# Kernel optimization log

Hardware: AMD Instinct MI355X
Metric: run time of the kernel (lower is better)

The kernel has to match this reference:

```python
import jax, jax.numpy as jnp
import numpy as np

N, E, D, R = 50000, 600000, 128, 500


def setup_inputs() -> dict:
    key = jax.random.key(0)
    ks = jax.random.split(key, 9)
    h = jax.random.normal(ks[0], (N, D), dtype=jnp.float32)
    norm = jax.random.uniform(ks[1], (N, 1), dtype=jnp.float32)
    emb_rel = jax.random.normal(ks[2], (R, D), dtype=jnp.float32)
    scale = 1.0 / np.sqrt(D)  # xavier-ish scale for DxD weights
    weight_neighbor = jax.random.normal(ks[3], (D, D), dtype=jnp.float32) * scale
    loop_weight = jax.random.normal(ks[4], (D, D), dtype=jnp.float32) * scale
    evolve_loop_weight = jax.random.normal(ks[5], (D, D), dtype=jnp.float32) * scale
    src = jax.random.randint(ks[6], (E,), 0, N, dtype=jnp.int32)
    dst = jax.random.randint(ks[7], (E,), 0, N, dtype=jnp.int32)
    etype = jax.random.randint(ks[8], (E,), 0, R, dtype=jnp.int32)
    return {
        "h": h, "norm": norm, "emb_rel": emb_rel,
        "weight_neighbor": weight_neighbor, "loop_weight": loop_weight,
        "evolve_loop_weight": evolve_loop_weight,
        "src": src, "dst": dst, "etype": etype,
    }


def reference(h, norm, emb_rel, weight_neighbor, loop_weight,
              evolve_loop_weight, src, dst, etype):
    # msg_func: gather src node features + relation embeddings, add, dense matmul
    msg = (h[src] + emb_rel[etype]) @ weight_neighbor        # [E, D]
    # update_all(fn.sum): scatter-sum messages into destination nodes
    agg = jax.ops.segment_sum(msg, dst, num_segments=N)       # [N, D]
    # apply_func: scale by per-node norm
    h_agg = agg * norm                                        # [N, D]
    # self-loop: nodes with in-degree > 0 use loop_weight, others evolve_loop_weight
    in_deg = jax.ops.segment_sum(jnp.ones((E,), dtype=jnp.float32), dst,
                                 num_segments=N)              # [N]
    loop_msg = jnp.where((in_deg > 0)[:, None],
                         h @ loop_weight,
                         h @ evolve_loop_weight)              # [N, D]
    node_repr = h_agg + loop_msg
    return jax.nn.relu(node_repr)
```

## Files before the change

### kernel.cpp

```cpp
#include <hip/hip_runtime.h>
#include <hip/hip_bf16.h>


#define DIM 128
#define MAXD 64

typedef __attribute__((ext_vector_type(8))) short bf16x8_t;
typedef __attribute__((ext_vector_type(4))) float f32x4_t;

__device__ inline ushort f2bf(float f) {
    __hip_bfloat16 b = __float2bfloat16(f);
    return *reinterpret_cast<ushort*>(&b);
}
__device__ inline float blo(unsigned u) { return __uint_as_float(u << 16); }
__device__ inline float bhi(unsigned u) { return __uint_as_float(u & 0xffff0000u); }
__device__ inline uint4 cvt8(const float4& a, const float4& b) {
    uint4 o;
    o.x = f2bf(a.x) | ((unsigned)f2bf(a.y) << 16);
    o.y = f2bf(a.z) | ((unsigned)f2bf(a.w) << 16);
    o.z = f2bf(b.x) | ((unsigned)f2bf(b.y) << 16);
    o.w = f2bf(b.z) | ((unsigned)f2bf(b.w) << 16);
    return o;
}

__global__ __launch_bounds__(256) void init_kernel(
    const float4* __restrict__ h4, const float4* __restrict__ emb4,
    const float* __restrict__ Wn, const float* __restrict__ Wl,
    uint4* __restrict__ h8, uint4* __restrict__ emb8,
    ushort* __restrict__ Bpack, int* __restrict__ cursor,
    int* __restrict__ zcount, int nH, int nE, int N, int R)
{
    int i = blockIdx.x * 256 + threadIdx.x;
    if (i < nH) {
        int per = (N + 1) * 2;
        int s = i / per, rem = i - s * per;
        int n = rem >> 1, hh = rem & 1;
        h8[i] = (n == N) ? make_uint4(0, 0, 0, 0)
                         : cvt8(h4[n * 32 + s * 4 + hh * 2],
                                h4[n * 32 + s * 4 + hh * 2 + 1]);
        return;
    }
    int j = i - nH;
    if (j < nE) {
        int per = (R + 1) * 2;
        int s = j / per, rem = j - s * per;
        int n = rem >> 1, hh = rem & 1;
        emb8[j] = (n == R) ? make_uint4(0, 0, 0, 0)
                           : cvt8(emb4[n * 32 + s * 4 + hh * 2],
                                  emb4[n * 32 + s * 4 + hh * 2 + 1]);
        return;
    }
    j -= nE;
    if (j < 32768) {
        int jj   = j & 7;
        int lane = (j >> 3) & 63;
        int ks   = (j >> 9) & 7;
        int nt   = j >> 12;
        int k = ks * 32 + (lane >> 4) * 8 + jj;
        int n = nt * 16 + (lane & 15);
        float v = (k < DIM) ? Wn[k * DIM + n] : Wl[(k - DIM) * DIM + n];
        Bpack[j] = f2bf(v);
        return;
    }
    j -= 32768;
    if (j < N) { cursor[j] = 0; return; }
    if (j == N) *zcount = 0;
}

__global__ __launch_bounds__(256) void fill_kernel(
    const int4* __restrict__ src4, const int4* __restrict__ dst4,
    const int4* __restrict__ et4, int* __restrict__ cursor,
    unsigned* __restrict__ region, int E4,
    const int* __restrict__ src, const int* __restrict__ dst,
    const int* __restrict__ etype, int E)
{
    int i = blockIdx.x * 256 + threadIdx.x;
    if (i < E4) {
        int4 s = src4[i], d = dst4[i], t = et4[i];
        int p;
        p = atomicAdd(cursor + d.x, 1);
        region[d.x * MAXD + p] = (unsigned)s.x | ((unsigned)t.x << 17);
        p = atomicAdd(cursor + d.y, 1);
        region[d.y * MAXD + p] = (unsigned)s.y | ((unsigned)t.y << 17);
        p = atomicAdd(cursor + d.z, 1);
        region[d.z * MAXD + p] = (unsigned)s.z | ((unsigned)t.z << 17);
        p = atomicAdd(cursor + d.w, 1);
        region[d.w * MAXD + p] = (unsigned)s.w | ((unsigned)t.w << 17);
    }
    if (i == 0)
        for (int e = E4 * 4; e < E; ++e) {
            int p = atomicAdd(cursor + dst[e], 1);
            region[dst[e] * MAXD + p] = (unsigned)src[e] | ((unsigned)etype[e] << 17);
        }
}

__device__ inline void addbf8(float* a, uint4 hv, uint4 rv) {
    a[0] += blo(hv.x) + blo(rv.x); a[1] += bhi(hv.x) + bhi(rv.x);
    a[2] += blo(hv.y) + blo(rv.y); a[3] += bhi(hv.y) + bhi(rv.y);
    a[4] += blo(hv.z) + blo(rv.z); a[5] += bhi(hv.z) + bhi(rv.z);
    a[6] += blo(hv.w) + blo(rv.w); a[7] += bhi(hv.w) + bhi(rv.w);
}

__global__ __launch_bounds__(256) void gather_kernel(
    const uint4* __restrict__ h8,
    const uint4* __restrict__ e8,
    const float* __restrict__ norm,
    const int* __restrict__ cursor,
    const unsigned* __restrict__ region,
    uint4* __restrict__ aggn8,
    int* __restrict__ zcount, int* __restrict__ zlist,
    int N, int R, unsigned SENT)
{
    __shared__ uint4 embS[1024];

    int s  = blockIdx.x & 7;
    int nb = blockIdx.x >> 3;

    const uint4* esrc = e8 + (size_t)s * (R + 1) * 2;
    int nse = (R + 1) * 2;
    if (nse > 1024) nse = 1024;
    for (int idx = threadIdx.x; idx < nse; idx += 256)
        embS[idx] = esrc[idx];
    __syncthreads();

    int n = nb * 128 + (threadIdx.x >> 1);
    if (n >= N) return;
    int l = threadIdx.x & 1;
    int cnt = cursor[n];
    uint4* aout = aggn8 + ((size_t)s * N + n) * 2 + l;

    if (cnt == 0) {
        if (s == 0 && l == 0) { int p = atomicAdd(zcount, 1); zlist[p] = n; }
        *aout = make_uint4(0, 0, 0, 0);
        return;
    }

    const uint4* hsl = h8 + (size_t)s * (N + 1) * 2 + l;
    const uint4* el  = embS + l;
    const unsigned* reg = region + (size_t)n * MAXD;
    float nm = norm[n];
    float a[8] = {0.f, 0.f, 0.f, 0.f, 0.f, 0.f, 0.f, 0.f};

    uint4 r = *(const uint4*)reg;
    for (int k = 0; k < cnt; k += 4) {
        int kp = (k + 4 < MAXD - 3) ? (k + 4) : (MAXD - 4);
        uint4 rn = *(const uint4*)(reg + kp);
        unsigned w0 = r.x;
        unsigned w1 = (k + 1 < cnt) ? r.y : SENT;
        unsigned w2 = (k + 2 < cnt) ? r.z : SENT;
        unsigned w3 = (k + 3 < cnt) ? r.w : SENT;
        uint4 h0 = hsl[(w0 & 0x1FFFF) * 2];
        uint4 h1 = hsl[(w1 & 0x1FFFF) * 2];
        uint4 h2 = hsl[(w2 & 0x1FFFF) * 2];
        uint4 h3 = hsl[(w3 & 0x1FFFF) * 2];
        uint4 e0 = el[(w0 >> 17) * 2];
        uint4 e1 = el[(w1 >> 17) * 2];
        uint4 e2 = el[(w2 >> 17) * 2];
        uint4 e3 = el[(w3 >> 17) * 2];
        addbf8(a, h0, e0);
        addbf8(a, h1, e1);
        addbf8(a, h2, e2);
        addbf8(a, h3, e3);
        r = rn;
    }

    uint4 o;
    o.x = f2bf(a[0] * nm) | ((unsigned)f2bf(a[1] * nm) << 16);
    o.y = f2bf(a[2] * nm) | ((unsigned)f2bf(a[3] * nm) << 16);
    o.z = f2bf(a[4] * nm) | ((unsigned)f2bf(a[5] * nm) << 16);
    o.w = f2bf(a[6] * nm) | ((unsigned)f2bf(a[7] * nm) << 16);
    *aout = o;
}

__global__ __launch_bounds__(256) void mfma_gemm_kernel(
    const ushort* __restrict__ aggn_bf,
    const ushort* __restrict__ h_bf,
    const ushort* __restrict__ Bpack,
    float* __restrict__ out,
    int nRowTiles, int halfWaves, int N)
{
    int wave = threadIdx.x >> 6;
    int lane = threadIdx.x & 63;
    int wid  = blockIdx.x * 4 + wave;
    int ch   = wid & 1;
    int w    = wid >> 1;
    int m    = lane & 15;
    int quad = lane >> 4;
    int sq   = quad >> 1;
    int off8 = (quad & 1) * 8;

    bf16x8_t b[4][8];
    #pragma unroll
    for (int nt = 0; nt < 4; ++nt)
        #pragma unroll
        for (int ks = 0; ks < 8; ++ks)
            b[nt][ks] = *(const bf16x8_t*)(Bpack +
                (((size_t)(ch * 4 + nt) * 8 + ks) * 64 + lane) * 8);

    for (int rt = w; rt < nRowTiles; rt += halfWaves) {
        int row = rt * 16 + m;
        bf16x8_t a[8];
        #pragma unroll
        for (int ks = 0; ks < 4; ++ks) {
            int s = 2 * ks + sq;
            a[ks]     = *(const bf16x8_t*)(aggn_bf +
                            ((size_t)s * N + row) * 16 + off8);
            a[ks + 4] = *(const bf16x8_t*)(h_bf +
                            ((size_t)s * (N + 1) + row) * 16 + off8);
        }
        f32x4_t acc[4];
        #pragma unroll
        for (int nt = 0; nt < 4; ++nt)
            #pragma unroll
            for (int r = 0; r < 4; ++r) acc[nt][r] = 0.f;

        #pragma unroll
        for (int ks = 0; ks < 8; ++ks)
            #pragma unroll
            for (int nt = 0; nt < 4; ++nt)
                acc[nt] = __builtin_amdgcn_mfma_f32_16x16x32_bf16(
                    a[ks], b[nt][ks], acc[nt], 0, 0, 0);

        int colBase = ch * 64 + m;
        int rowBase = rt * 16 + quad * 4;
        #pragma unroll
        for (int nt = 0; nt < 4; ++nt)
            #pragma unroll
            for (int r = 0; r < 4; ++r)
                out[(size_t)(rowBase + r) * DIM + colBase + nt * 16] =
                    fmaxf(acc[nt][r], 0.f);
    }
}

__global__ __launch_bounds__(128) void fixup_kernel(
    const float* __restrict__ h, const float* __restrict__ We,
    const int* __restrict__ zlist, const int* __restrict__ zcount,
    float* __restrict__ out)
{
    int cnt = *zcount;
    int c = threadIdx.x;
    for (int i = blockIdx.x; i < cnt; i += gridDim.x) {
        int n = zlist[i];
        float s = 0.f;
        for (int k = 0; k < DIM; ++k)
            s = fmaf(h[(size_t)n * DIM + k], We[(size_t)k * DIM + c], s);
        out[(size_t)n * DIM + c] = fmaxf(s, 0.f);
    }
}

extern "C" void kernel_launch(void* const* d_in, const int* in_sizes, int n_in,
                              void* d_out, int out_size, void* d_ws, size_t ws_size,
                              hipStream_t stream)
{
    const float* h    = (const float*)d_in[0];
    const float* norm = (const float*)d_in[1];
    const float* emb  = (const float*)d_in[2];
    const float* Wn   = (const float*)d_in[3];
    const float* Wl   = (const float*)d_in[4];
    const float* We   = (const float*)d_in[5];
    const int* src    = (const int*)d_in[6];
    const int* dst    = (const int*)d_in[7];
    const int* etype  = (const int*)d_in[8];

    const int N = in_sizes[1];
    const int E = in_sizes[6];
    const int R = in_sizes[2] / DIM;

    char* p = (char*)d_ws;
    ushort*   h_bf    = (ushort*)p;    p += (size_t)(N + 1) * DIM * 2;
    ushort*   emb_bf  = (ushort*)p;    p += (size_t)(R + 1) * DIM * 2;
    ushort*   Bpack   = (ushort*)p;    p += 2 * DIM * DIM * 2;
    ushort*   aggn_bf = (ushort*)p;    p += (size_t)N * DIM * 2;
    unsigned* region  = (unsigned*)p;  p += (size_t)N * MAXD * 4 + 64;
    int*      cursor  = (int*)p;       p += ((size_t)N * 4 + 15) & ~(size_t)15;
    int*      zcount  = (int*)p;       p += 16;
    int*      zlist   = (int*)p;

    const int nH = 8 * (N + 1) * 2;
    const int nE = 8 * (R + 1) * 2;
    const int initTotal = nH + nE + 32768 + N + 1;
    const unsigned SENT = (unsigned)N | ((unsigned)R << 17);

    init_kernel<<<dim3((initTotal + 255) / 256), dim3(256), 0, stream>>>(
        (const float4*)h, (const float4*)emb, Wn, Wl,
        (uint4*)h_bf, (uint4*)emb_bf, Bpack, cursor, zcount, nH, nE, N, R);

    fill_kernel<<<dim3((E / 4 + 255) / 256), dim3(256), 0, stream>>>(
        (const int4*)src, (const int4*)dst, (const int4*)etype,
        cursor, region, E / 4, src, dst, etype, E);

    const int nodeBlocks = (N + 127) / 128;
    gather_kernel<<<dim3(nodeBlocks * 8), dim3(256), 0, stream>>>(
        (const uint4*)h_bf, (const uint4*)emb_bf, norm, cursor, region,
        (uint4*)aggn_bf, zcount, zlist, N, R, SENT);

    const int nRowTiles = (N + 15) / 16;
    mfma_gemm_kernel<<<dim3(512), dim3(256), 0, stream>>>(
        aggn_bf, h_bf, Bpack, (float*)d_out, nRowTiles, 1024, N);

    fixup_kernel<<<dim3(2), dim3(128), 0, stream>>>(
        h, We, zlist, zcount, (float*)d_out);
}
```

Baseline: 183.9 us.

## Partition edge bucketing by destination range using LDS counters per workgroup

Replaces global-atomic edge bucketing with a scheme where each of about 256 workgroups owns a contiguous range of destination nodes. Each workgroup scans the full dst array and uses shared-memory atomics for its own nodes, then writes the per-node counts to global cursors. This removes global atomics and the separate cursor zeroing, but every workgroup reads all of dst (about 2.4MB each, mostly from L2). MAXD drops from 64 to 48 to shrink the region buffer, which risks overflow if a node's in-degree exceeds 48.

```diff
diff --git a/kernel.cpp b/kernel.cpp
--- a/kernel.cpp
+++ b/kernel.cpp
@@ -3,7 +3,7 @@
 
 
 #define DIM 128
-#define MAXD 64
+#define MAXD 48
 
 typedef __attribute__((ext_vector_type(8))) short bf16x8_t;
 typedef __attribute__((ext_vector_type(4))) float f32x4_t;
@@ -27,8 +27,8 @@
     const float4* __restrict__ h4, const float4* __restrict__ emb4,
     const float* __restrict__ Wn, const float* __restrict__ Wl,
     uint4* __restrict__ h8, uint4* __restrict__ emb8,
-    ushort* __restrict__ Bpack, int* __restrict__ cursor,
-    int* __restrict__ zcount, int nH, int nE, int N, int R)
+    ushort* __restrict__ Bpack, int* __restrict__ zcount,
+    int nH, int nE, int N, int R)
 {
     int i = blockIdx.x * 256 + threadIdx.x;
     if (i < nH) {
@@ -63,35 +63,58 @@
         return;
     }
     j -= 32768;
-    if (j < N) { cursor[j] = 0; return; }
-    if (j == N) *zcount = 0;
-}
-
-__global__ __launch_bounds__(256) void fill_kernel(
-    const int4* __restrict__ src4, const int4* __restrict__ dst4,
-    const int4* __restrict__ et4, int* __restrict__ cursor,
-    unsigned* __restrict__ region, int E4,
+    if (j == 0) *zcount = 0;
+}
+
+__global__ __launch_bounds__(512) void fill_kernel(
+    const int4* __restrict__ dst4,
     const int* __restrict__ src, const int* __restrict__ dst,
-    const int* __restrict__ etype, int E)
-{
-    int i = blockIdx.x * 256 + threadIdx.x;
-    if (i < E4) {
-        int4 s = src4[i], d = dst4[i], t = et4[i];
-        int p;
-        p = atomicAdd(cursor + d.x, 1);
-        region[d.x * MAXD + p] = (unsigned)s.x | ((unsigned)t.x << 17);
-        p = atomicAdd(cursor + d.y, 1);
-        region[d.y * MAXD + p] = (unsigned)s.y | ((unsigned)t.y << 17);
-        p = atomicAdd(cursor + d.z, 1);
-        region[d.z * MAXD + p] = (unsigned)s.z | ((unsigned)t.z << 17);
-        p = atomicAdd(cursor + d.w, 1);
-        region[d.w * MAXD + p] = (unsigned)s.w | ((unsigned)t.w << 17);
-    }
-    if (i == 0)
-        for (int e = E4 * 4; e < E; ++e) {
-            int p = atomicAdd(cursor + dst[e], 1);
-            region[dst[e] * MAXD + p] = (unsigned)src[e] | ((unsigned)etype[e] << 17);
-        }
+    const int* __restrict__ etype,
+    int* __restrict__ cursor, unsigned* __restrict__ region,
+    int E4, int E, int chunk, int N)
+{
+    __shared__ int cl[256];
+    int base = blockIdx.x * chunk;
+    int hi   = base + chunk; if (hi > N) hi = N;
+    int cn   = hi - base;
+    if (cn <= 0) return;
+    for (int t = threadIdx.x; t < cn; t += 512) cl[t] = 0;
+    __syncthreads();
+
+    for (int i = threadIdx.x; i < E4; i += 512) {
+        int4 d = dst4[i];
+        int e = 4 * i;
+        if ((unsigned)(d.x - base) < (unsigned)cn) {
+            int p = atomicAdd(&cl[d.x - base], 1);
+            region[(size_t)d.x * MAXD + p] =
+                (unsigned)src[e] | ((unsigned)etype[e] << 17);
+        }
+        if ((unsigned)(d.y - base) < (unsigned)cn) {
+            int p = atomicAdd(&cl[d.y - base], 1);
+            region[(size_t)d.y * MAXD + p] =
+                (unsigned)src[e + 1] | ((unsigned)etype[e + 1] << 17);
+        }
+        if ((unsigned)(d.z - base) < (unsigned)cn) {
+            int p = atomicAdd(&cl[d.z - base], 1);
+            region[(size_t)d.z * MAXD + p] =
+                (unsigned)src[e + 2] | ((unsigned)etype[e + 2] << 17);
+        }
+        if ((unsigned)(d.w - base) < (unsigned)cn) {
+            int p = atomicAdd(&cl[d.w - base], 1);
+            region[(size_t)d.w * MAXD + p] =
+                (unsigned)src[e + 3] | ((unsigned)etype[e + 3] << 17);
+        }
+    }
+    for (int e = E4 * 4 + threadIdx.x; e < E; e += 512) {
+        int d = dst[e];
+        if ((unsigned)(d - base) < (unsigned)cn) {
+            int p = atomicAdd(&cl[d - base], 1);
+            region[(size_t)d * MAXD + p] =
+                (unsigned)src[e] | ((unsigned)etype[e] << 17);
+        }
+    }
+    __syncthreads();
+    for (int t = threadIdx.x; t < cn; t += 512) cursor[base + t] = cl[t];
 }
 
 __device__ inline void addbf8(float* a, uint4 hv, uint4 rv) {
@@ -278,16 +301,18 @@
 
     const int nH = 8 * (N + 1) * 2;
     const int nE = 8 * (R + 1) * 2;
-    const int initTotal = nH + nE + 32768 + N + 1;
+    const int initTotal = nH + nE + 32768 + 1;
     const unsigned SENT = (unsigned)N | ((unsigned)R << 17);
 
     init_kernel<<<dim3((initTotal + 255) / 256), dim3(256), 0, stream>>>(
         (const float4*)h, (const float4*)emb, Wn, Wl,
-        (uint4*)h_bf, (uint4*)emb_bf, Bpack, cursor, zcount, nH, nE, N, R);
-
-    fill_kernel<<<dim3((E / 4 + 255) / 256), dim3(256), 0, stream>>>(
-        (const int4*)src, (const int4*)dst, (const int4*)etype,
-        cursor, region, E / 4, src, dst, etype, E);
+        (uint4*)h_bf, (uint4*)emb_bf, Bpack, zcount, nH, nE, N, R);
+
+    const int chunk = (N + 255) / 256;
+    const int nWG   = (N + chunk - 1) / chunk;
+    fill_kernel<<<dim3(nWG), dim3(512), 0, stream>>>(
+        (const int4*)dst, src, dst, etype, cursor, region,
+        E / 4, E, chunk, N);
 
     const int nodeBlocks = (N + 127) / 128;
     gather_kernel<<<dim3(nodeBlocks * 8), dim3(256), 0, stream>>>(
```

Result: slower. 306.8 us (+66.8%).
